# Kernel optimization log

Hardware: AMD Instinct MI355X
Metric: run time of the kernel (lower is better)

## Reference

```python
import jax, jax.numpy as jnp
import numpy as np

N_NODES = 100000


def gcn_conv(x, src, dst, W, b, n_nodes):
    # GCNConv: h = x @ W, then symmetric-normalized aggregation (self-loops already in src/dst)
    h = x @ W  # [N, out]
    ones = jnp.ones(src.shape[0], dtype=h.dtype)
    deg = jax.ops.segment_sum(ones, dst, num_segments=n_nodes)  # in-degree incl. self-loop
    dinv = jnp.where(deg > 0, jax.lax.rsqrt(deg), 0.0)
    norm = dinv[src] * dinv[dst]  # [E]
    msg = h[src] * norm[:, None]  # [E, out] gather
    out = jax.ops.segment_sum(msg, dst, num_segments=n_nodes)  # scatter-add
    return out + b


def setup_inputs() -> dict:
    key = jax.random.key(0)
    k1, k2, k3, k4 = jax.random.split(key, 4)
    n, f, h, c, e = N_NODES, 256, 128, 40, 1600000
    x = jax.random.normal(k1, (n, f), dtype=jnp.float32)
    edge_index = jax.random.randint(k2, (2, e), 0, n, dtype=jnp.int64)
    W1 = jax.random.normal(k3, (f, h), dtype=jnp.float32) * (1.0 / np.sqrt(f))
    b1 = jnp.zeros((h,), dtype=jnp.float32)
    W2 = jax.random.normal(k4, (h, c), dtype=jnp.float32) * (1.0 / np.sqrt(h))
    b2 = jnp.zeros((c,), dtype=jnp.float32)
    return {"x": x, "edge_index": edge_index, "W1": W1, "b1": b1, "W2": W2, "b2": b2}


def reference(x, edge_index, W1, b1, W2, b2):
    n = x.shape[0]
    loops = jnp.arange(n, dtype=edge_index.dtype)
    src = jnp.concatenate([edge_index[0], loops])
    dst = jnp.concatenate([edge_index[1], loops])
    h = jax.nn.relu(gcn_conv(x, src, dst, W1, b1, n))
    # dropout is identity in eval mode (self.training == False)
    logits = gcn_conv(h, src, dst, W2, b2, n)
    return jax.nn.log_softmax(logits, axis=1)
```

## Files before the change

### kernel.cpp

```cpp
#include <hip/hip_runtime.h>
#include <hip/hip_fp16.h>
#include <math.h>

#define FIN 256
#define HID 128
#define NCLS 40
#define ZPB 64
#define BKT_SHIFT 9
#define BKT_SZ 512
#define CHUNK 2048
#define CAP 12288

typedef __attribute__((ext_vector_type(8))) short short8_t;
typedef __attribute__((ext_vector_type(8))) _Float16 half8_t;
typedef __attribute__((ext_vector_type(4))) float f32x4;
typedef __attribute__((ext_vector_type(2))) float f32x2;

static __device__ __forceinline__ ushort f2bf(float f) {
    unsigned u = __float_as_uint(f);
    u += 0x7FFF + ((u >> 16) & 1);
    return (ushort)(u >> 16);
}

static __device__ __forceinline__ unsigned pack_ew(int s, float w) {
    return ((unsigned)s << 15) | (__float_as_uint(w) >> 17);
}



__global__ void k_prep(int* __restrict__ bcur, const float* __restrict__ W1,
                       ushort* __restrict__ Wt, const float* __restrict__ W2,
                       __half* __restrict__ W2t, int nbk) {
    int i = blockIdx.x * 256 + threadIdx.x;
    if (i <= nbk) bcur[i] = 0;
    if (i < FIN * HID) {
        int c = i >> 8, k = i & 255;
        Wt[i] = f2bf(W1[(size_t)k * HID + c]);
    }
    if (i < 48 * HID) {
        int c = i >> 7, p = i & 127;
        int k = (p & 7) * 16 + (p >> 3);
        W2t[i] = __float2half((c < NCLS) ? W2[(size_t)k * NCLS + c] : 0.f);
    }
}


__global__ __launch_bounds__(256) void k_g1bkt(const float* __restrict__ X,
                                               const ushort* __restrict__ Wt,
                                               unsigned char* __restrict__ H8, int M,
                                               const int* __restrict__ src,
                                               const int* __restrict__ dst, int E,
                                               int* __restrict__ bcur,
                                               unsigned* __restrict__ ebkt,
                                               int nbk, int nbkb) {
    __shared__ uint4 wlds[64 * 32];
    int tid = threadIdx.x;
    int b = (int)blockIdx.x;
    bool is_bkt = ((b % 3) == 0) && (b / 3 < nbkb);

    if (is_bkt) {
        int bkb = b / 3;
        int* hist  = (int*)wlds;
        int* scanb = hist + 256;
        int* base  = scanb + 256;
        int* gbase = base + 256;
        unsigned* stage = (unsigned*)(gbase + 256);
        unsigned char* sbk = (unsigned char*)(stage + CHUNK);
        int e0 = bkb * CHUNK;
        int cntc = min(CHUNK, E - e0);
        hist[tid] = 0;
        __syncthreads();

        int s_[8], d_[8], bk_[8], rk_[8];
#pragma unroll
        for (int i = 0; i < 8; i++) {
            int j = tid + i * 256;
            if (j < cntc) {
                int s = src[e0 + j], d = dst[e0 + j];
                s_[i] = s; d_[i] = d;
                bk_[i] = d >> BKT_SHIFT;
                rk_[i] = atomicAdd(&hist[bk_[i]], 1);
            } else {
                bk_[i] = -1;
            }
        }
        __syncthreads();

        scanb[tid] = hist[tid];
        __syncthreads();
        for (int o = 1; o < 256; o <<= 1) {
            int u = (tid >= o) ? scanb[tid - o] : 0;
            __syncthreads();
            scanb[tid] += u;
            __syncthreads();
        }
        base[tid] = scanb[tid] - hist[tid];
        if (tid < nbk && hist[tid] > 0) gbase[tid] = atomicAdd(&bcur[tid], hist[tid]);
        __syncthreads();

#pragma unroll
        for (int i = 0; i < 8; i++) {
            if (bk_[i] >= 0) {
                int p = base[bk_[i]] + rk_[i];
                stage[p] = ((unsigned)s_[i] << 9) | ((unsigned)d_[i] & 511u);
                sbk[p] = (unsigned char)bk_[i];
            }
        }
        __syncthreads();

#pragma unroll
        for (int i = 0; i < 8; i++) {
            int j = tid + i * 256;
            if (j < cntc) {
                int bk = sbk[j];
                ebkt[(size_t)bk * CAP + gbase[bk] + (j - base[bk])] = stage[j];
            }
        }
        return;
    }

    int bid = b - b / 3 - ((b % 3) ? 1 : 0);
    if (b % 3 == 0) bid = nbkb * 2 + (b / 3 - nbkb);
    int wid = tid >> 6, lane = tid & 63;
    int q = lane & 15, kg = lane >> 4;
    int grow_in = bid * 64 + wid * 16 + q;
    int lrow = min(grow_in, M - 1);
    const float* xr = X + (size_t)lrow * FIN;

    float4 xf0[8], xf1[8];
#pragma unroll
    for (int kt = 0; kt < 8; kt++) {
        int k0 = kt * 32 + kg * 8;
        xf0[kt] = *(const float4*)(xr + k0);
        xf1[kt] = *(const float4*)(xr + k0 + 4);
    }

    short8_t a[8];
#pragma unroll
    for (int kt = 0; kt < 8; kt++) {
        unsigned r0, r1, r2, r3;
        asm("v_cvt_pk_bf16_f32 %0, %1, %2" : "=v"(r0) : "v"(xf0[kt].x), "v"(xf0[kt].y));
        asm("v_cvt_pk_bf16_f32 %0, %1, %2" : "=v"(r1) : "v"(xf0[kt].z), "v"(xf0[kt].w));
        asm("v_cvt_pk_bf16_f32 %0, %1, %2" : "=v"(r2) : "v"(xf1[kt].x), "v"(xf1[kt].y));
        asm("v_cvt_pk_bf16_f32 %0, %1, %2" : "=v"(r3) : "v"(xf1[kt].z), "v"(xf1[kt].w));
        union { uint4 u; short8_t s; } cv;
        cv.u = make_uint4(r0, r1, r2, r3);
        a[kt] = cv.s;
    }

    f32x4 accA[4], accB[4];
#pragma unroll
    for (int c = 0; c < 4; c++) {
        accA[c] = (f32x4){0.f, 0.f, 0.f, 0.f};
        accB[c] = (f32x4){0.f, 0.f, 0.f, 0.f};
    }

    const uint4* wg = (const uint4*)Wt;
#pragma unroll
    for (int h = 0; h < 2; h++) {
        if (h) __syncthreads();
#pragma unroll
        for (int i = 0; i < 8; i++) {
            int e = tid + i * 256;
            int lc = e >> 5, ch = e & 31;
            wlds[lc * 32 + (ch ^ (lc & 7))] = wg[(size_t)h * 2048 + e];
        }
        __syncthreads();

        f32x4* acc = h ? accB : accA;
#pragma unroll
        for (int kt = 0; kt < 8; kt++) {
            int ch = kt * 4 + kg;
#pragma unroll
            for (int c = 0; c < 4; c++) {
                int lc = c * 16 + q;
                short8_t bfr = *(const short8_t*)&wlds[lc * 32 + (ch ^ (lc & 7))];
                acc[c] = __builtin_amdgcn_mfma_f32_16x16x32_bf16(a[kt], bfr, acc[c], 0, 0, 0);
            }
        }
    }

#pragma unroll
    for (int i = 0; i < 4; i++) {
        int r = bid * 64 + wid * 16 + kg * 4 + i;
        if (r < M) {
            int lo = 0, hi = 0;
            lo = __builtin_amdgcn_cvt_pk_fp8_f32(accA[0][i], accA[1][i], lo, false);
            lo = __builtin_amdgcn_cvt_pk_fp8_f32(accA[2][i], accA[3][i], lo, true);
            hi = __builtin_amdgcn_cvt_pk_fp8_f32(accB[0][i], accB[1][i], hi, false);
            hi = __builtin_amdgcn_cvt_pk_fp8_f32(accB[2][i], accB[3][i], hi, true);
            *(uint2*)(H8 + (size_t)r * HID + q * 8) = make_uint2((unsigned)lo, (unsigned)hi);
        }
    }
}


__global__ __launch_bounds__(512) void k_cnt(const unsigned* __restrict__ ebkt,
                                             int* __restrict__ bcur, int nbk,
                                             int* __restrict__ off, int* __restrict__ cnt,
                                             float* __restrict__ dinv, int n) {
    __shared__ int lcnt[BKT_SZ];
    __shared__ int lofs[BKT_SZ];
    __shared__ int lbase;
    int b = blockIdx.x, t = threadIdx.x;
    int n0 = b << BKT_SHIFT;
    lcnt[t] = 0;
    __syncthreads();
    int sz = bcur[b];
    const unsigned* ep = ebkt + (size_t)b * CAP;
    for (int e = t; e < sz; e += 512) atomicAdd(&lcnt[ep[e] & 511u], 1);
    __syncthreads();
    if (t == 0) lbase = atomicAdd(&bcur[nbk], sz);
    lofs[t] = lcnt[t];
    __syncthreads();
    for (int o = 1; o < 512; o <<= 1) {
        int u = (t >= o) ? lofs[t - o] : 0;
        __syncthreads();
        lofs[t] += u;
        __syncthreads();
    }
    int node = n0 + t;
    if (node < n) {
        int c = lcnt[t];
        off[node] = lbase + lofs[t] - c;
        cnt[node] = c;
        dinv[node] = rsqrtf((float)(c + 1));
    }
}


__global__ __launch_bounds__(512) void k_place(const unsigned* __restrict__ ebkt,
                                               const int* __restrict__ bcur,
                                               const int* __restrict__ off,
                                               const float* __restrict__ dinv,
                                               unsigned* __restrict__ eew, int n) {
    __shared__ int curx[BKT_SZ];
    __shared__ float ldin[BKT_SZ];
    int b = blockIdx.x, t = threadIdx.x;
    int n0 = b << BKT_SHIFT;
    int node = n0 + t;
    if (node < n) {
        curx[t] = off[node];
        ldin[t] = dinv[node];
    }
    __syncthreads();
    int sz = bcur[b];
    const unsigned* ep = ebkt + (size_t)b * CAP;
    for (int e = t; e < sz; e += 512) {
        unsigned ed = ep[e];
        int s = (int)(ed >> 9), dl = (int)(ed & 511u);
        float w = dinv[s] * ldin[dl];
        int pos = atomicAdd(&curx[dl], 1);
        eew[pos] = pack_ew(s, w);
    }
}


__global__ __launch_bounds__(256) void k_agg1(const unsigned char* __restrict__ H8,
                                              const unsigned* __restrict__ eew,
                                              const int* __restrict__ off,
                                              const int* __restrict__ cnt,
                                              const float* __restrict__ dinv,
                                              const float* __restrict__ b1,
                                              __half* __restrict__ H2, int n) {
    int tid = threadIdx.x;
    int node = blockIdx.x * 16 + (tid >> 4);
    int q = tid & 15;
    if (node >= n) return;
    float di = dinv[node];
    int start = off[node], ne = cnt[node];

    float acc[8];
    {
        uint2 v = *(const uint2*)(H8 + (size_t)node * HID + q * 8);
        float wv = di * di;
        f32x2 f;
        f = __builtin_amdgcn_cvt_pk_f32_fp8((int)v.x, false);
        acc[0] = f[0] * wv; acc[1] = f[1] * wv;
        f = __builtin_amdgcn_cvt_pk_f32_fp8((int)v.x, true);
        acc[2] = f[0] * wv; acc[3] = f[1] * wv;
        f = __builtin_amdgcn_cvt_pk_f32_fp8((int)v.y, false);
        acc[4] = f[0] * wv; acc[5] = f[1] * wv;
        f = __builtin_amdgcn_cvt_pk_f32_fp8((int)v.y, true);
        acc[6] = f[0] * wv; acc[7] = f[1] * wv;
    }

#pragma unroll 4
    for (int j = 0; j < ne; ++j) {
        unsigned u = eew[start + j];
        int s = (int)(u >> 15);
        float wv = __uint_as_float((u & 0x7FFFu) << 17);
        uint2 v = *(const uint2*)(H8 + (size_t)s * HID + q * 8);
        f32x2 f;
        f = __builtin_amdgcn_cvt_pk_f32_fp8((int)v.x, false);
        acc[0] = fmaf(f[0], wv, acc[0]); acc[1] = fmaf(f[1], wv, acc[1]);
        f = __builtin_amdgcn_cvt_pk_f32_fp8((int)v.x, true);
        acc[2] = fmaf(f[0], wv, acc[2]); acc[3] = fmaf(f[1], wv, acc[3]);
        f = __builtin_amdgcn_cvt_pk_f32_fp8((int)v.y, false);
        acc[4] = fmaf(f[0], wv, acc[4]); acc[5] = fmaf(f[1], wv, acc[5]);
        f = __builtin_amdgcn_cvt_pk_f32_fp8((int)v.y, true);
        acc[6] = fmaf(f[0], wv, acc[6]); acc[7] = fmaf(f[1], wv, acc[7]);
    }

    float r[8];
#pragma unroll
    for (int i = 0; i < 8; i++) r[i] = fmaxf(acc[i] + b1[i * 16 + q], 0.f);
    __half2 p0 = __floats2half2_rn(r[0], r[1]);
    __half2 p1 = __floats2half2_rn(r[2], r[3]);
    __half2 p2 = __floats2half2_rn(r[4], r[5]);
    __half2 p3 = __floats2half2_rn(r[6], r[7]);
    uint4 o4;
    o4.x = *(unsigned*)&p0; o4.y = *(unsigned*)&p1;
    o4.z = *(unsigned*)&p2; o4.w = *(unsigned*)&p3;
    *(uint4*)(H2 + (size_t)node * HID + q * 8) = o4;
}


__global__ __launch_bounds__(256) void k_gemm2(const __half* __restrict__ H2,
                                               const __half* __restrict__ W2t,
                                               unsigned char* __restrict__ Z8, int M) {
    int tid = threadIdx.x;
    int wid = tid >> 6, lane = tid & 63;
    int q = lane & 15, kg = lane >> 4;
    int row = blockIdx.x * 64 + wid * 16 + q;
    int lrow = min(row, M - 1);
    const __half* hr = H2 + (size_t)lrow * HID;

    half8_t a[4];
#pragma unroll
    for (int kt = 0; kt < 4; kt++) a[kt] = *(const half8_t*)(hr + kt * 32 + kg * 8);

    f32x4 acc[3];
#pragma unroll
    for (int c = 0; c < 3; c++) acc[c] = (f32x4){0.f, 0.f, 0.f, 0.f};

#pragma unroll
    for (int c = 0; c < 3; c++) {
        const __half* wc = W2t + (size_t)(c * 16 + q) * HID + kg * 8;
#pragma unroll
        for (int kt = 0; kt < 4; kt++) {
            half8_t b = *(const half8_t*)(wc + kt * 32);
            acc[c] = __builtin_amdgcn_mfma_f32_16x16x32_f16(a[kt], b, acc[c], 0, 0, 0);
        }
    }

    int r0 = blockIdx.x * 64 + wid * 16 + kg * 4;
#pragma unroll
    for (int c = 0; c < 3; c++) {
        int col = c * 16 + q;
        if (col < NCLS) {
#pragma unroll
            for (int i = 0; i < 4; i++) {
                int r = r0 + i;
                if (r < M) {
                    int p = __builtin_amdgcn_cvt_pk_fp8_f32(acc[c][i], acc[c][i], 0, false);
                    Z8[(size_t)r * ZPB + col] = (unsigned char)(p & 0xff);
                }
            }
        }
    }
}


__global__ __launch_bounds__(256) void k_agg2(const unsigned char* __restrict__ Z8,
                                              const unsigned* __restrict__ eew,
                                              const int* __restrict__ off,
                                              const int* __restrict__ cnt,
                                              const float* __restrict__ dinv,
                                              const float* __restrict__ b2,
                                              float* __restrict__ Out, int n) {
    int tid = threadIdx.x;
    int node = blockIdx.x * 32 + (tid >> 3);
    int l = tid & 7;
    if (node >= n) return;
    float di = dinv[node];
    int start = off[node], ne = cnt[node];

    float acc[8];
    {
        uint2 v = *(const uint2*)(Z8 + (size_t)node * ZPB + l * 8);
        float wv = di * di;
        f32x2 f;
        f = __builtin_amdgcn_cvt_pk_f32_fp8((int)v.x, false);
        acc[0] = f[0] * wv; acc[1] = f[1] * wv;
        f = __builtin_amdgcn_cvt_pk_f32_fp8((int)v.x, true);
        acc[2] = f[0] * wv; acc[3] = f[1] * wv;
        f = __builtin_amdgcn_cvt_pk_f32_fp8((int)v.y, false);
        acc[4] = f[0] * wv; acc[5] = f[1] * wv;
        f = __builtin_amdgcn_cvt_pk_f32_fp8((int)v.y, true);
        acc[6] = f[0] * wv; acc[7] = f[1] * wv;
    }

#pragma unroll 4
    for (int j = 0; j < ne; ++j) {
        unsigned u = eew[start + j];
        int s = (int)(u >> 15);
        float wv = __uint_as_float((u & 0x7FFFu) << 17);
        uint2 v = *(const uint2*)(Z8 + (size_t)s * ZPB + l * 8);
        f32x2 f;
        f = __builtin_amdgcn_cvt_pk_f32_fp8((int)v.x, false);
        acc[0] = fmaf(f[0], wv, acc[0]); acc[1] = fmaf(f[1], wv, acc[1]);
        f = __builtin_amdgcn_cvt_pk_f32_fp8((int)v.x, true);
        acc[2] = fmaf(f[0], wv, acc[2]); acc[3] = fmaf(f[1], wv, acc[3]);
        f = __builtin_amdgcn_cvt_pk_f32_fp8((int)v.y, false);
        acc[4] = fmaf(f[0], wv, acc[4]); acc[5] = fmaf(f[1], wv, acc[5]);
        f = __builtin_amdgcn_cvt_pk_f32_fp8((int)v.y, true);
        acc[6] = fmaf(f[0], wv, acc[6]); acc[7] = fmaf(f[1], wv, acc[7]);
    }

    bool valid = (l < 5);
    float v[8];
    float m = -INFINITY;
#pragma unroll
    for (int i = 0; i < 8; i++) {
        v[i] = valid ? acc[i] + b2[l * 8 + i] : -INFINITY;
        m = fmaxf(m, v[i]);
    }
#pragma unroll
    for (int o = 1; o <= 4; o <<= 1) m = fmaxf(m, __shfl_xor(m, o));
    float ssum = 0.f;
#pragma unroll
    for (int i = 0; i < 8; i++)
        if (valid) ssum += __expf(v[i] - m);
#pragma unroll
    for (int o = 1; o <= 4; o <<= 1) ssum += __shfl_xor(ssum, o);
    float lse = m + logf(ssum);

    if (valid) {
        float4 w0 = make_float4(v[0] - lse, v[1] - lse, v[2] - lse, v[3] - lse);
        float4 w1 = make_float4(v[4] - lse, v[5] - lse, v[6] - lse, v[7] - lse);
        float* op = Out + (size_t)node * NCLS + l * 8;
        *(float4*)op = w0;
        *(float4*)(op + 4) = w1;
    }
}


extern "C" void kernel_launch(void* const* d_in, const int* in_sizes, int n_in,
                              void* d_out, int out_size, void* d_ws, size_t ws_size,
                              hipStream_t stream) {
    const float* x  = (const float*)d_in[0];
    const int* ei   = (const int*)d_in[1];
    const float* W1 = (const float*)d_in[2];
    const float* b1 = (const float*)d_in[3];
    const float* W2 = (const float*)d_in[4];
    const float* b2 = (const float*)d_in[5];
    float* out = (float*)d_out;

    const int n = in_sizes[0] / FIN;
    const int E = in_sizes[1] / 2;
    const int* src = ei;
    const int* dst = ei + E;
    const int nbk = (n + BKT_SZ - 1) >> BKT_SHIFT;

    char* w = (char*)d_ws;
    auto alloc = [&](size_t bytes) {
        char* p = w;
        w += (bytes + 255) & ~(size_t)255;
        return p;
    };
    int* off     = (int*)alloc((size_t)n * 4);
    int* cnt     = (int*)alloc((size_t)n * 4);
    float* dinv  = (float*)alloc((size_t)n * 4);
    int* bcur    = (int*)alloc((size_t)(nbk + 1) * 4);
    unsigned* ebkt = (unsigned*)alloc((size_t)nbk * CAP * 4);
    unsigned* eew  = (unsigned*)alloc((size_t)E * 4);
    ushort* wt   = (ushort*)alloc((size_t)FIN * HID * 2);
    __half* w2t  = (__half*)alloc((size_t)48 * HID * 2);
    unsigned char* H8 = (unsigned char*)alloc((size_t)n * HID);
    __half* H2   = (__half*)alloc((size_t)n * HID * 2);
    unsigned char* Z8 = (unsigned char*)alloc((size_t)n * ZPB);

    const int nbkb = (E + CHUNK - 1) / CHUNK;
    const int g1b = (n + 63) / 64;

    k_prep<<<(FIN * HID) / 256, 256, 0, stream>>>(bcur, W1, wt, W2, w2t, nbk);

    k_g1bkt<<<nbkb + g1b, 256, 0, stream>>>(x, wt, H8, n, src, dst, E, bcur, ebkt, nbk, nbkb);

    k_cnt<<<nbk, 512, 0, stream>>>(ebkt, bcur, nbk, off, cnt, dinv, n);
    k_place<<<nbk, 512, 0, stream>>>(ebkt, bcur, off, dinv, eew, n);

    k_agg1<<<(n + 15) / 16, 256, 0, stream>>>(H8, eew, off, cnt, dinv, b1, H2, n);

    k_gemm2<<<(n + 63) / 64, 256, 0, stream>>>(H2, w2t, Z8, n);
    k_agg2<<<(n + 31) / 32, 256, 0, stream>>>(Z8, eew, off, cnt, dinv, b2, out, n);
}
```

Baseline: 146.5 us.

## Fuse second-layer GEMM into first aggregation kernel via shared memory

The layer-1 aggregation kernel now stages its 16 ReLU'd fp16 node rows in shared memory and has one wavefront run the MFMA product with W2, writing fp8 Z8 directly. This removes the separate k_gemm2 launch and the global H2 round trip, about 25.6 MB of writes plus reads. The cost is a block-wide barrier and a serial MFMA tail done by only 64 of 256 threads per block, which may hurt latency hiding in this gather-bound kernel. Out-of-range nodes are clamped instead of returning early, so every thread reaches the barrier.

```diff
diff --git a/kernel.cpp b/kernel.cpp
--- a/kernel.cpp
+++ b/kernel.cpp
@@ -262,17 +262,19 @@
                                               const int* __restrict__ cnt,
                                               const float* __restrict__ dinv,
                                               const float* __restrict__ b1,
-                                              __half* __restrict__ H2, int n) {
+                                              const __half* __restrict__ W2t,
+                                              unsigned char* __restrict__ Z8, int n) {
+    __shared__ __half h2s[16][136];
     int tid = threadIdx.x;
-    int node = blockIdx.x * 16 + (tid >> 4);
-    int q = tid & 15;
-    if (node >= n) return;
-    float di = dinv[node];
-    int start = off[node], ne = cnt[node];
+    int g = tid >> 4, q = tid & 15;
+    int node = blockIdx.x * 16 + g;
+    int nodec = min(node, n - 1);
+    float di = dinv[nodec];
+    int start = off[nodec], ne = cnt[nodec];
 
     float acc[8];
     {
-        uint2 v = *(const uint2*)(H8 + (size_t)node * HID + q * 8);
+        uint2 v = *(const uint2*)(H8 + (size_t)nodec * HID + q * 8);
         float wv = di * di;
         f32x2 f;
         f = __builtin_amdgcn_cvt_pk_f32_fp8((int)v.x, false);
@@ -312,49 +314,42 @@
     uint4 o4;
     o4.x = *(unsigned*)&p0; o4.y = *(unsigned*)&p1;
     o4.z = *(unsigned*)&p2; o4.w = *(unsigned*)&p3;
-    *(uint4*)(H2 + (size_t)node * HID + q * 8) = o4;
-}
-
-
-__global__ __launch_bounds__(256) void k_gemm2(const __half* __restrict__ H2,
-                                               const __half* __restrict__ W2t,
-                                               unsigned char* __restrict__ Z8, int M) {
-    int tid = threadIdx.x;
-    int wid = tid >> 6, lane = tid & 63;
-    int q = lane & 15, kg = lane >> 4;
-    int row = blockIdx.x * 64 + wid * 16 + q;
-    int lrow = min(row, M - 1);
-    const __half* hr = H2 + (size_t)lrow * HID;
-
-    half8_t a[4];
-#pragma unroll
-    for (int kt = 0; kt < 4; kt++) a[kt] = *(const half8_t*)(hr + kt * 32 + kg * 8);
-
-    f32x4 acc[3];
-#pragma unroll
-    for (int c = 0; c < 3; c++) acc[c] = (f32x4){0.f, 0.f, 0.f, 0.f};
-
-#pragma unroll
-    for (int c = 0; c < 3; c++) {
-        const __half* wc = W2t + (size_t)(c * 16 + q) * HID + kg * 8;
-#pragma unroll
-        for (int kt = 0; kt < 4; kt++) {
-            half8_t b = *(const half8_t*)(wc + kt * 32);
-            acc[c] = __builtin_amdgcn_mfma_f32_16x16x32_f16(a[kt], b, acc[c], 0, 0, 0);
-        }
-    }
-
-    int r0 = blockIdx.x * 64 + wid * 16 + kg * 4;
-#pragma unroll
-    for (int c = 0; c < 3; c++) {
-        int col = c * 16 + q;
-        if (col < NCLS) {
-#pragma unroll
-            for (int i = 0; i < 4; i++) {
-                int r = r0 + i;
-                if (r < M) {
-                    int p = __builtin_amdgcn_cvt_pk_fp8_f32(acc[c][i], acc[c][i], 0, false);
-                    Z8[(size_t)r * ZPB + col] = (unsigned char)(p & 0xff);
+    *(uint4*)&h2s[g][q * 8] = o4;
+    __syncthreads();
+
+    if (tid < 64) {
+        int qq = tid & 15, kg = tid >> 4;
+        half8_t a[4];
+#pragma unroll
+        for (int kt = 0; kt < 4; kt++)
+            a[kt] = *(const half8_t*)&h2s[qq][kt * 32 + kg * 8];
+
+        f32x4 zacc[3];
+#pragma unroll
+        for (int c = 0; c < 3; c++) zacc[c] = (f32x4){0.f, 0.f, 0.f, 0.f};
+
+#pragma unroll
+        for (int c = 0; c < 3; c++) {
+            const __half* wc = W2t + (size_t)(c * 16 + qq) * HID + kg * 8;
+#pragma unroll
+            for (int kt = 0; kt < 4; kt++) {
+                half8_t bfr = *(const half8_t*)(wc + kt * 32);
+                zacc[c] = __builtin_amdgcn_mfma_f32_16x16x32_f16(a[kt], bfr, zacc[c], 0, 0, 0);
+            }
+        }
+
+        int rbase = blockIdx.x * 16 + kg * 4;
+#pragma unroll
+        for (int c = 0; c < 3; c++) {
+            int col = c * 16 + qq;
+            if (col < NCLS) {
+#pragma unroll
+                for (int i = 0; i < 4; i++) {
+                    int rr = rbase + i;
+                    if (rr < n) {
+                        int p = __builtin_amdgcn_cvt_pk_fp8_f32(zacc[c][i], zacc[c][i], 0, false);
+                        Z8[(size_t)rr * ZPB + col] = (unsigned char)(p & 0xff);
+                    }
                 }
             }
         }
@@ -468,7 +463,6 @@
     ushort* wt   = (ushort*)alloc((size_t)FIN * HID * 2);
     __half* w2t  = (__half*)alloc((size_t)48 * HID * 2);
     unsigned char* H8 = (unsigned char*)alloc((size_t)n * HID);
-    __half* H2   = (__half*)alloc((size_t)n * HID * 2);
     unsigned char* Z8 = (unsigned char*)alloc((size_t)n * ZPB);
 
     const int nbkb = (E + CHUNK - 1) / CHUNK;
@@ -481,8 +475,7 @@
     k_cnt<<<nbk, 512, 0, stream>>>(ebkt, bcur, nbk, off, cnt, dinv, n);
     k_place<<<nbk, 512, 0, stream>>>(ebkt, bcur, off, dinv, eew, n);
 
-    k_agg1<<<(n + 15) / 16, 256, 0, stream>>>(H8, eew, off, cnt, dinv, b1, H2, n);
-
-    k_gemm2<<<(n + 63) / 64, 256, 0, stream>>>(H2, w2t, Z8, n);
+    k_agg1<<<(n + 15) / 16, 256, 0, stream>>>(H8, eew, off, cnt, dinv, b1, w2t, Z8, n);
+
     k_agg2<<<(n + 31) / 32, 256, 0, stream>>>(Z8, eew, off, cnt, dinv, b2, out, n);
 }
```

New measurement: 137.2 us (median of 2 runs). 1.07x faster.
